# Optimization experiments

Measured on AMD Instinct MI355X. Metric: run time of the kernel, lower is better.

## Reference

```python
import jax, jax.numpy as jnp
import numpy as np

N, E, IN, HID, H, C, L, G = 20000, 640000, 128, 256, 8, 32, 5, 64
NEG_SLOPE = 0.2


def _layernorm(x, g, b, eps=1e-5):
    mu = jnp.mean(x, axis=-1, keepdims=True)
    var = jnp.mean((x - mu) ** 2, axis=-1, keepdims=True)
    return (x - mu) * jax.lax.rsqrt(var + eps) * g + b


def _gatv2(h, src, dst, Wl, bl, Wr, br, att, out_bias):
    # h: [N, HID]; src/dst: [E+N] (self loops appended)
    n = h.shape[0]
    xl = (h @ Wl + bl).reshape(n, H, C)  # source transform
    xr = (h @ Wr + br).reshape(n, H, C)  # target transform
    e = jax.nn.leaky_relu(xl[src] + xr[dst], NEG_SLOPE)       # [Etot, H, C]
    logits = jnp.einsum('ehc,hc->eh', e, att)                  # [Etot, H]
    m = jax.ops.segment_max(logits, dst, num_segments=n)       # segment softmax over dst
    a = jnp.exp(logits - m[dst])
    s = jax.ops.segment_sum(a, dst, num_segments=n)
    alpha = a / (s[dst] + 1e-16)                               # [Etot, H]
    out = jax.ops.segment_sum(alpha[:, :, None] * xl[src], dst, num_segments=n)
    return out.reshape(n, HID) + out_bias


def setup_inputs() -> dict:
    key = jax.random.key(0)
    ks = jax.random.split(key, 16)
    sc = 0.05
    inp = {
        'x': jax.random.normal(ks[0], (N, IN), jnp.float32),
        'edge_index': jax.random.randint(ks[1], (2, E), 0, N, jnp.int64),
        'batch': jnp.sort(jax.random.randint(ks[2], (N,), 0, G, jnp.int64)),
        'proj_W': jax.random.normal(ks[3], (IN, HID), jnp.float32) * sc,
        'proj_b': jnp.zeros((HID,), jnp.float32),
        'Wl': jax.random.normal(ks[4], (L, HID, HID), jnp.float32) * sc,
        'bl': jnp.zeros((L, HID), jnp.float32),
        'Wr': jax.random.normal(ks[5], (L, HID, HID), jnp.float32) * sc,
        'br': jnp.zeros((L, HID), jnp.float32),
        'att': jax.random.normal(ks[6], (L, H, C), jnp.float32) * sc,
        'out_bias': jnp.zeros((L, HID), jnp.float32),
        'ln_g': jnp.ones((L, HID), jnp.float32),
        'ln_b': jnp.zeros((L, HID), jnp.float32),
    }
    return inp


def reference(x, edge_index, batch, proj_W, proj_b, Wl, bl, Wr, br, att, out_bias, ln_g, ln_b):
    n = x.shape[0]
    loops = jnp.arange(n, dtype=edge_index.dtype)
    src = jnp.concatenate([edge_index[0], loops])  # add_self_loops=True
    dst = jnp.concatenate([edge_index[1], loops])
    h = x @ proj_W + proj_b
    for i in range(L):  # dropout = identity in eval mode
        conv = _gatv2(h, src, dst, Wl[i], bl[i], Wr[i], br[i], att[i], out_bias[i])
        h = _layernorm(h + jax.nn.elu(conv), ln_g[i], ln_b[i])
    counts = jax.ops.segment_sum(jnp.ones((n,), h.dtype), batch, num_segments=G)
    gsum = jax.ops.segment_sum(h, batch, num_segments=G)
    graph_emb = gsum / jnp.maximum(counts, 1.0)[:, None]  # global_mean_pool
    return graph_emb, h, batch
```

## Files before the change

### kernel.cpp

```cpp
#include <hip/hip_runtime.h>
#include <hip/hip_bf16.h>

#define NN   20000
#define NE   640000
#define INF_ 128
#define HID  256
#define NL   5
#define NG   64

typedef __hip_bfloat16 bf16;
typedef __attribute__((ext_vector_type(4))) float f32x4;
typedef __attribute__((ext_vector_type(8))) short bf16x8;

#if __has_builtin(__builtin_amdgcn_exp2f)
#define EXP2F __builtin_amdgcn_exp2f
#else
#define EXP2F exp2f
#endif

__device__ __forceinline__ float b2f(bf16 v) { return __bfloat162float(v); }
__device__ __forceinline__ short f2bs(float v) {
  union { bf16 h; short s; } u; u.h = __float2bfloat16(v); return u.s;
}
__device__ __forceinline__ f32x4 ldbf4o(const char* __restrict__ basep, unsigned off) {
  const uint2 u = *(const uint2*)(basep + off);
  f32x4 r;
  r[0] = __uint_as_float(u.x << 16);
  r[1] = __uint_as_float(u.x & 0xffff0000u);
  r[2] = __uint_as_float(u.y << 16);
  r[3] = __uint_as_float(u.y & 0xffff0000u);
  return r;
}

#if __has_builtin(__builtin_amdgcn_update_dpp)
template<int CTRL>
__device__ __forceinline__ float dpp_add(float v) {
  int t = __builtin_amdgcn_update_dpp(0, __float_as_int(v), CTRL, 0xF, 0xF, true);
  return v + __int_as_float(t);
}
__device__ __forceinline__ float hsum8(float v) {
  v = dpp_add<0xB1>(v);
  v = dpp_add<0x4E>(v);
  v = dpp_add<0x141>(v);
  return v;
}
__device__ __forceinline__ float wsum64(float v) {
  v = hsum8(v);
  v = dpp_add<0x140>(v);
  v += __shfl_xor(v, 16);
  v += __shfl_xor(v, 32);
  return v;
}
#else
__device__ __forceinline__ float hsum8(float v) {
  v += __shfl_xor(v, 1);  v += __shfl_xor(v, 2);  v += __shfl_xor(v, 4);
  return v;
}
__device__ __forceinline__ float wsum64(float v) {
  v += __shfl_xor(v, 1);  v += __shfl_xor(v, 2);  v += __shfl_xor(v, 4);
  v += __shfl_xor(v, 8);  v += __shfl_xor(v, 16); v += __shfl_xor(v, 32);
  return v;
}
#endif

__global__ void detect_kernel(const int* __restrict__ ei,
                              const int* __restrict__ batch,
                              int* __restrict__ flags) {
  if (blockIdx.x == 0) {
    const int k = threadIdx.x;
    const bool e_bad = (k < 40) && (ei[2 * (k * 15999) + 1] != 0);
    const bool b_bad = (k < 40) && (batch[2 * (k * 249) + 1] != 0);
    const int e64 = __any(e_bad) ? 0 : 1;
    const int b64 = __any(b_bad) ? 0 : 1;
    if (k == 0) { flags[0] = e64; flags[1] = b64; }
  }
}

__device__ __forceinline__ int ld_i(const int* p, int f, size_t idx) {
  return f ? p[2 * idx] : p[idx];
}

__global__ void hist_kernel(const int* __restrict__ ei, const int* __restrict__ flags,
                            int* __restrict__ deg) {
  int e = blockIdx.x * blockDim.x + threadIdx.x;
  if (e >= NE) return;
  int f = flags[0];
  int d = ld_i(ei, f, (size_t)NE + e);
  if ((unsigned)d < NN) atomicAdd(&deg[d], 1);
}

#define SCAN_NB ((NN + 255) / 256)
__global__ __launch_bounds__(256) void scan1_kernel(
    const int* __restrict__ deg, int* __restrict__ off, int* __restrict__ bsum)
{
  __shared__ int sh[256];
  const int t = threadIdx.x;
  const int i = blockIdx.x * 256 + t;
  const int v = (i < NN) ? deg[i] : 0;
  sh[t] = v;
  __syncthreads();
  for (int d = 1; d < 256; d <<= 1) {
    int nv = (t >= d) ? sh[t - d] : 0;
    __syncthreads();
    sh[t] += nv;
    __syncthreads();
  }
  if (i < NN) off[i] = sh[t] - v;
  if (t == 255) bsum[blockIdx.x] = sh[255];
}

__global__ __launch_bounds__(128) void scan2_kernel(
    const int* __restrict__ bsum, int* __restrict__ boff, int* __restrict__ off)
{
  __shared__ int sh[128];
  const int t = threadIdx.x;
  const int v = (t < SCAN_NB) ? bsum[t] : 0;
  sh[t] = v;
  __syncthreads();
  for (int d = 1; d < 128; d <<= 1) {
    int nv = (t >= d) ? sh[t - d] : 0;
    __syncthreads();
    sh[t] += nv;
    __syncthreads();
  }
  if (t < SCAN_NB) boff[t] = sh[t] - v;
  if (t == SCAN_NB - 1) off[NN] = sh[t];
}

__global__ __launch_bounds__(256) void scan3_kernel(
    int* __restrict__ off, const int* __restrict__ boff, int* __restrict__ tmp)
{
  const int i = blockIdx.x * 256 + threadIdx.x;
  if (i < NN) {
    const int val = off[i] + boff[blockIdx.x];
    off[i] = val;
    tmp[i] = val;
  }
}

__global__ void scatter_kernel(const int* __restrict__ ei, const int* __restrict__ flags,
                               int* __restrict__ tmp, int* __restrict__ csr) {
  int e = blockIdx.x * blockDim.x + threadIdx.x;
  if (e >= NE) return;
  int f = flags[0];
  int d = ld_i(ei, f, (size_t)NE + e);
  int s = ld_i(ei, f, (size_t)e);
  if ((unsigned)d < NN) {
    int p = atomicAdd(&tmp[d], 1);
    int sv = ((unsigned)s < NN) ? s : 0;
    if ((unsigned)p < NE) csr[p] = sv * (HID * 2);
  }
}

__global__ __launch_bounds__(256) void prep_bt_kernel(
    const float* __restrict__ projW, const float* __restrict__ Wl,
    const float* __restrict__ Wr, short* __restrict__ BTp,
    short* __restrict__ BTl, short* __restrict__ BTr)
{
  __shared__ float t[32][33];
  const int z = blockIdx.z;
  const float* src; short* dst; int K;
  if (z == 0)      { src = projW;                            dst = BTp;                              K = INF_; }
  else if (z <= NL){ src = Wl + (size_t)(z - 1) * HID * HID; dst = BTl + (size_t)(z - 1) * HID * HID; K = HID; }
  else             { src = Wr + (size_t)(z - 1 - NL) * HID * HID; dst = BTr + (size_t)(z - 1 - NL) * HID * HID; K = HID; }
  const int k0 = blockIdx.y * 32;
  if (k0 >= K) return;
  const int n0 = blockIdx.x * 32;
  const int tx = threadIdx.x & 31;
  const int ty = threadIdx.x >> 5;
#pragma unroll
  for (int i = 0; i < 32; i += 8)
    t[ty + i][tx] = src[(size_t)(k0 + ty + i) * HID + n0 + tx];
  __syncthreads();
#pragma unroll
  for (int i = 0; i < 32; i += 8)
    dst[(size_t)(n0 + ty + i) * K + k0 + tx] = f2bs(t[tx][ty + i]);
}

template<int K, bool A_BF16>
__global__ __launch_bounds__(256) void gemm_bias_kernel(
    const void* __restrict__ Av, const float* __restrict__ B,
    const float* __restrict__ bias, float* __restrict__ Cf,
    bf16* __restrict__ Cb, int M)
{
  constexpr int N = 256;
  constexpr int LDB = K + 8;
  __shared__ __align__(16) short bT[32 * LDB];
  const int tid = threadIdx.x;
  const int n0 = blockIdx.x * 32;
  const int m_base = blockIdx.y * 256;

  if (tid < K) {
    const float* brow = B + (size_t)tid * N + n0;
#pragma unroll
    for (int j = 0; j < 32; ++j) bT[j * LDB + tid] = f2bs(brow[j]);
  }
  __syncthreads();

  const int wave = tid >> 6;
  const int lane = tid & 63;
  const int r    = lane & 15;
  const int quad = lane >> 4;
  const int m_wave = m_base + wave * 64;

  f32x4 acc[4][2];
#pragma unroll
  for (int i = 0; i < 4; ++i) { acc[i][0] = (f32x4)0.0f; acc[i][1] = (f32x4)0.0f; }

#pragma unroll
  for (int kk = 0; kk < K / 32; ++kk) {
    const int kof = kk * 32 + quad * 8;
    bf16x8 b0 = *(const bf16x8*)&bT[r * LDB + kof];
    bf16x8 b1 = *(const bf16x8*)&bT[(r + 16) * LDB + kof];
#pragma unroll
    for (int sm = 0; sm < 4; ++sm) {
      const int row = m_wave + sm * 16 + r;
      bf16x8 a = (bf16x8)(short)0;
      if (row < M) {
        if constexpr (A_BF16) {
          a = *(const bf16x8*)((const short*)Av + (size_t)row * K + kof);
        } else {
          const float* ap = (const float*)Av + (size_t)row * K + kof;
          f32x4 lo = *(const f32x4*)ap;
          f32x4 hi = *(const f32x4*)(ap + 4);
#pragma unroll
          for (int j = 0; j < 4; ++j) { a[j] = f2bs(lo[j]); a[4 + j] = f2bs(hi[j]); }
        }
      }
      acc[sm][0] = __builtin_amdgcn_mfma_f32_16x16x32_bf16(a, b0, acc[sm][0], 0, 0, 0);
      acc[sm][1] = __builtin_amdgcn_mfma_f32_16x16x32_bf16(a, b1, acc[sm][1], 0, 0, 0);
    }
  }

  const float bv0 = bias[n0 + r];
  const float bv1 = bias[n0 + 16 + r];
#pragma unroll
  for (int sm = 0; sm < 4; ++sm) {
#pragma unroll
    for (int rg = 0; rg < 4; ++rg) {
      const int row = m_wave + sm * 16 + quad * 4 + rg;
      if (row < M) {
        size_t i0 = (size_t)row * N + n0 + r;
        float v0 = acc[sm][0][rg] + bv0;
        float v1 = acc[sm][1][rg] + bv1;
        if (Cf) { Cf[i0] = v0; Cf[i0 + 16] = v1; }
        if (Cb) {
          ((unsigned short*)Cb)[i0]      = (unsigned short)f2bs(v0);
          ((unsigned short*)Cb)[i0 + 16] = (unsigned short)f2bs(v1);
        }
      }
    }
  }
}

template<bool A_BF16>
__global__ __launch_bounds__(256) void gemm_dual_kernel(
    const void* __restrict__ Av,
    const float* __restrict__ Bl, const float* __restrict__ Br,
    const float* __restrict__ bl, const float* __restrict__ br,
    bf16* __restrict__ Cl, bf16* __restrict__ Cr, int M)
{
  constexpr int K = HID, N = 256;
  constexpr int LDB = K + 8;
  __shared__ __align__(16) short bTl[32 * LDB];
  __shared__ __align__(16) short bTr[32 * LDB];
  const int tid = threadIdx.x;
  const int n0 = blockIdx.x * 32;
  const int m_base = blockIdx.y * 256;

  {
    const float* browl = Bl + (size_t)tid * N + n0;
    const float* browr = Br + (size_t)tid * N + n0;
#pragma unroll
    for (int j = 0; j < 32; ++j) {
      bTl[j * LDB + tid] = f2bs(browl[j]);
      bTr[j * LDB + tid] = f2bs(browr[j]);
    }
  }
  __syncthreads();

  const int wave = tid >> 6;
  const int lane = tid & 63;
  const int r    = lane & 15;
  const int quad = lane >> 4;
  const int m_wave = m_base + wave * 64;

  f32x4 accl[4][2], accr[4][2];
#pragma unroll
  for (int i = 0; i < 4; ++i) {
    accl[i][0] = (f32x4)0.0f; accl[i][1] = (f32x4)0.0f;
    accr[i][0] = (f32x4)0.0f; accr[i][1] = (f32x4)0.0f;
  }

#pragma unroll
  for (int kk = 0; kk < K / 32; ++kk) {
    const int kof = kk * 32 + quad * 8;
    bf16x8 b0l = *(const bf16x8*)&bTl[r * LDB + kof];
    bf16x8 b1l = *(const bf16x8*)&bTl[(r + 16) * LDB + kof];
    bf16x8 b0r = *(const bf16x8*)&bTr[r * LDB + kof];
    bf16x8 b1r = *(const bf16x8*)&bTr[(r + 16) * LDB + kof];
#pragma unroll
    for (int sm = 0; sm < 4; ++sm) {
      const int row = m_wave + sm * 16 + r;
      bf16x8 a = (bf16x8)(short)0;
      if (row < M) {
        if constexpr (A_BF16) {
          a = *(const bf16x8*)((const short*)Av + (size_t)row * K + kof);
        } else {
          const float* ap = (const float*)Av + (size_t)row * K + kof;
          f32x4 lo = *(const f32x4*)ap;
          f32x4 hi = *(const f32x4*)(ap + 4);
#pragma unroll
          for (int j = 0; j < 4; ++j) { a[j] = f2bs(lo[j]); a[4 + j] = f2bs(hi[j]); }
        }
      }
      accl[sm][0] = __builtin_amdgcn_mfma_f32_16x16x32_bf16(a, b0l, accl[sm][0], 0, 0, 0);
      accl[sm][1] = __builtin_amdgcn_mfma_f32_16x16x32_bf16(a, b1l, accl[sm][1], 0, 0, 0);
      accr[sm][0] = __builtin_amdgcn_mfma_f32_16x16x32_bf16(a, b0r, accr[sm][0], 0, 0, 0);
      accr[sm][1] = __builtin_amdgcn_mfma_f32_16x16x32_bf16(a, b1r, accr[sm][1], 0, 0, 0);
    }
  }

  const float bl0v = bl[n0 + r],  bl1v = bl[n0 + 16 + r];
  const float br0v = br[n0 + r],  br1v = br[n0 + 16 + r];
#pragma unroll
  for (int sm = 0; sm < 4; ++sm) {
#pragma unroll
    for (int rg = 0; rg < 4; ++rg) {
      const int row = m_wave + sm * 16 + quad * 4 + rg;
      if (row < M) {
        size_t i0 = (size_t)row * N + n0 + r;
        ((unsigned short*)Cl)[i0]      = (unsigned short)f2bs(accl[sm][0][rg] + bl0v);
        ((unsigned short*)Cl)[i0 + 16] = (unsigned short)f2bs(accl[sm][1][rg] + bl1v);
        ((unsigned short*)Cr)[i0]      = (unsigned short)f2bs(accr[sm][0][rg] + br0v);
        ((unsigned short*)Cr)[i0 + 16] = (unsigned short)f2bs(accr[sm][1][rg] + br1v);
      }
    }
  }
}

__global__ __launch_bounds__(256) void gemm_dual_tiled_kernel(
    const short* __restrict__ Ab,
    const short* __restrict__ BTl, const short* __restrict__ BTr,
    const float* __restrict__ bl, const float* __restrict__ br,
    bf16* __restrict__ Cl, bf16* __restrict__ Cr, int M)
{
  constexpr int K = HID;
  __shared__ __align__(16) short bfr[32768];
  const int tid  = threadIdx.x;
  const int lane = tid & 63;
  const int wv   = tid >> 6;
  const int bx   = blockIdx.x;
  const int n0   = (bx & 1) * 128;
  const short* BT = (bx < 2) ? BTl : BTr;
  const float* bias = (bx < 2) ? bl : br;
  bf16* C = (bx < 2) ? Cl : Cr;

#pragma unroll
  for (int it = 0; it < 16; ++it) {
    const int c  = it * 256 + tid;
    const int f  = c >> 6;
    const int ln = c & 63;
    const int nf = f >> 3, kk = f & 7;
    const int rr = ln & 15, qq = ln >> 4;
    const short* src = BT + (size_t)(n0 + nf * 16 + rr) * K + kk * 32 + qq * 8;
    *(bf16x8*)&bfr[(size_t)c * 8] = *(const bf16x8*)src;
  }
  __syncthreads();

  const int r    = lane & 15;
  const int quad = lane >> 4;
  const int m_wave = blockIdx.y * 128 + wv * 32;

  f32x4 acc[2][8];
#pragma unroll
  for (int sm = 0; sm < 2; ++sm)
#pragma unroll
    for (int nf = 0; nf < 8; ++nf) acc[sm][nf] = (f32x4)0.0f;

  const int ar0 = min(m_wave + r, M - 1);
  const int ar1 = min(m_wave + 16 + r, M - 1);
  const short* a0p = Ab + (size_t)ar0 * K + quad * 8;
  const short* a1p = Ab + (size_t)ar1 * K + quad * 8;
#pragma unroll
  for (int kk = 0; kk < 8; ++kk) {
    const bf16x8 a0 = *(const bf16x8*)(a0p + kk * 32);
    const bf16x8 a1 = *(const bf16x8*)(a1p + kk * 32);
#pragma unroll
    for (int nf = 0; nf < 8; ++nf) {
      const bf16x8 b = *(const bf16x8*)&bfr[((nf * 8 + kk) * 64 + lane) * 8];
      acc[0][nf] = __builtin_amdgcn_mfma_f32_16x16x32_bf16(a0, b, acc[0][nf], 0, 0, 0);
      acc[1][nf] = __builtin_amdgcn_mfma_f32_16x16x32_bf16(a1, b, acc[1][nf], 0, 0, 0);
    }
  }

  float bv[8];
#pragma unroll
  for (int nf = 0; nf < 8; ++nf) bv[nf] = bias[n0 + nf * 16 + r];

#pragma unroll
  for (int sm = 0; sm < 2; ++sm) {
#pragma unroll
    for (int rg = 0; rg < 4; ++rg) {
      const int row = m_wave + sm * 16 + quad * 4 + rg;
      if (row < M) {
        unsigned short* cp = (unsigned short*)C + (size_t)row * 256 + n0 + r;
#pragma unroll
        for (int nf = 0; nf < 8; ++nf)
          cp[nf * 16] = (unsigned short)f2bs(acc[sm][nf][rg] + bv[nf]);
      }
    }
  }
}

__global__ __launch_bounds__(256) void gat_layer_kernel(
    const bf16* __restrict__ xl, const bf16* __restrict__ xr,
    float* __restrict__ h, bf16* __restrict__ h_bf,
    const int* __restrict__ off, const int* __restrict__ csr,
    const float* __restrict__ att, const float* __restrict__ outb,
    const float* __restrict__ lng, const float* __restrict__ lnb)
{
  const int lane = threadIdx.x & 63;
  const int node = __builtin_amdgcn_readfirstlane(blockIdx.x * 4 + (threadIdx.x >> 6));
  const int cb   = ((lane >> 3) << 5) + ((lane & 7) << 2);
  const unsigned cb2  = (unsigned)cb * 2;
  const unsigned selfo = (unsigned)node * (HID * 2) + cb2;
  const size_t base = (size_t)node * HID + cb;
  const char* xlc = (const char*)xl;

  const f32x4 xrv = ldbf4o((const char*)xr, selfo);
  const f32x4 xls = ldbf4o(xlc, selfo);
  const f32x4 av = *(const f32x4*)(att + cb);
  f32x4 a6, a4;
#pragma unroll
  for (int c = 0; c < 4; ++c) {
    a6[c] = av[c] * (0.6f * 1.44269504f);
    a4[c] = av[c] * (0.4f * 1.44269504f);
  }

  const f32x4 ob = *(const f32x4*)(outb + cb);
  const f32x4 hv = *(const f32x4*)(h + base);
  const f32x4 g4 = *(const f32x4*)(lng + cb);
  const f32x4 b4 = *(const f32x4*)(lnb + cb);

  float pa = 0.f;
#pragma unroll
  for (int c = 0; c < 4; ++c) {
    float z = xls[c] + xrv[c];
    pa = fmaf(a6[c], z, pa);
    pa = fmaf(a4[c], fabsf(z), pa);
  }
  const float es = EXP2F(hsum8(pa));
  float s = es;
  f32x4 o;
#pragma unroll
  for (int c = 0; c < 4; ++c) o[c] = es * xls[c];

  int beg = __builtin_amdgcn_readfirstlane(off[node]);
  int end = __builtin_amdgcn_readfirstlane(off[node + 1]);
  if (beg < 0) beg = 0;
  if (end > NE) end = NE;
  const unsigned* csrb = (const unsigned*)csr;

  const int nblk = (end > beg) ? ((end - beg) >> 3) : 0;
  unsigned nx[8];
  if (nblk > 0) {
#pragma unroll
    for (int j = 0; j < 8; ++j) nx[j] = csrb[beg + j];
  }
  for (int b = 0; b < nblk; ++b) {
    f32x4 xv[8];
#pragma unroll
    for (int j = 0; j < 8; ++j) xv[j] = ldbf4o(xlc, nx[j] + cb2);
    if (b + 1 < nblk) {
      const int pn = beg + (b + 1) * 8;
#pragma unroll
      for (int j = 0; j < 8; ++j) nx[j] = csrb[pn + j];
    }
    float e[8];
#pragma unroll
    for (int j = 0; j < 8; ++j) {
      float acc = 0.f;
#pragma unroll
      for (int c = 0; c < 4; ++c) {
        float z = xv[j][c] + xrv[c];
        acc = fmaf(a6[c], z, acc);
        acc = fmaf(a4[c], fabsf(z), acc);
      }
      e[j] = EXP2F(hsum8(acc));
    }
    s += (((e[0] + e[1]) + (e[2] + e[3])) + ((e[4] + e[5]) + (e[6] + e[7])));
#pragma unroll
    for (int c = 0; c < 4; ++c) {
      float c0 = fmaf(e[0], xv[0][c], fmaf(e[1], xv[1][c],
                 fmaf(e[2], xv[2][c], fmaf(e[3], xv[3][c], o[c]))));
      float c1 = fmaf(e[4], xv[4][c], fmaf(e[5], xv[5][c],
                 fmaf(e[6], xv[6][c], e[7] * xv[7][c])));
      o[c] = c0 + c1;
    }
  }
  for (int p = beg + nblk * 8; p < end; ++p) {
    const unsigned oo = csrb[p] + cb2;
    const f32x4 xv = ldbf4o(xlc, oo);
    float pe = 0.f;
#pragma unroll
    for (int c = 0; c < 4; ++c) {
      float z = xv[c] + xrv[c];
      pe = fmaf(a6[c], z, pe);
      pe = fmaf(a4[c], fabsf(z), pe);
    }
    const float ee = EXP2F(hsum8(pe));
    s += ee;
#pragma unroll
    for (int c = 0; c < 4; ++c) o[c] = fmaf(ee, xv[c], o[c]);
  }

  const float inv_s = 1.f / s;
  f32x4 res;
#pragma unroll
  for (int c = 0; c < 4; ++c) {
    float conv = fmaf(o[c], inv_s, ob[c]);
    float el = conv > 0.f ? conv : (__expf(conv) - 1.f);
    res[c] = hv[c] + el;
  }
  float pr = (res[0] + res[1]) + (res[2] + res[3]);
  const float mu = wsum64(pr) * (1.f / 256.f);
  f32x4 dv;
  float p2s = 0.f;
#pragma unroll
  for (int c = 0; c < 4; ++c) { dv[c] = res[c] - mu; p2s = fmaf(dv[c], dv[c], p2s); }
  const float var = wsum64(p2s) * (1.f / 256.f);
  const float rs = rsqrtf(var + 1e-5f);
  f32x4 y;
#pragma unroll
  for (int c = 0; c < 4; ++c) y[c] = fmaf(dv[c] * rs, g4[c], b4[c]);

  *(f32x4*)(h + base) = y;
  if (h_bf) {
    ushort4 u;
    u.x = (unsigned short)f2bs(y[0]);
    u.y = (unsigned short)f2bs(y[1]);
    u.z = (unsigned short)f2bs(y[2]);
    u.w = (unsigned short)f2bs(y[3]);
    *(ushort4*)((unsigned short*)h_bf + base) = u;
  }
}

__global__ __launch_bounds__(256) void pool_kernel(
    const float* __restrict__ h, const int* __restrict__ batch,
    const int* __restrict__ flags, float* __restrict__ gsum, int* __restrict__ gcnt)
{
  const int t = threadIdx.x;
  const int f = flags[1];
  int n0 = blockIdx.x * 80;
  int n1 = n0 + 80; if (n1 > NN) n1 = NN;
  float acc = 0.f;
  int g_cur = ld_i(batch, f, n0);
  if ((unsigned)g_cur >= NG) g_cur = 0;
  int run = 0;
  for (int n = n0; n < n1; ++n) {
    int g = ld_i(batch, f, n);
    if ((unsigned)g >= NG) g = 0;
    if (g != g_cur) {
      atomicAdd(&gsum[(size_t)g_cur * HID + t], acc);
      if (t == 0) atomicAdd(&gcnt[g_cur], run);
      acc = 0.f; run = 0; g_cur = g;
    }
    acc += h[(size_t)n * HID + t];
    ++run;
  }
  atomicAdd(&gsum[(size_t)g_cur * HID + t], acc);
  if (t == 0) atomicAdd(&gcnt[g_cur], run);
}

__global__ void write_out_kernel(const float* __restrict__ gsum, const int* __restrict__ gcnt,
                                 const int* __restrict__ batch,
                                 const int* __restrict__ flags, float* __restrict__ out)
{
  int i = blockIdx.x * blockDim.x + threadIdx.x;
  if (i < NG * HID) {
    int g = i >> 8;
    float c = (float)gcnt[g];
    c = c > 1.f ? c : 1.f;
    out[i] = gsum[i] / c;
  } else if (i < NG * HID + NN) {
    int n = i - NG * HID;
    int f = flags[1];
    out[(size_t)NG * HID + (size_t)NN * HID + n] = (float)ld_i(batch, f, (size_t)n);
  }
}

extern "C" void kernel_launch(void* const* d_in, const int* in_sizes, int n_in,
                              void* d_out, int out_size, void* d_ws, size_t ws_size,
                              hipStream_t stream) {
  (void)in_sizes; (void)n_in; (void)out_size;

  const float* x     = (const float*)d_in[0];
  const int*   ei    = (const int*)d_in[1];
  const int*   batch = (const int*)d_in[2];
  const float* projW = (const float*)d_in[3];
  const float* projB = (const float*)d_in[4];
  const float* Wl    = (const float*)d_in[5];
  const float* bl    = (const float*)d_in[6];
  const float* Wr    = (const float*)d_in[7];
  const float* br    = (const float*)d_in[8];
  const float* att   = (const float*)d_in[9];
  const float* outb  = (const float*)d_in[10];
  const float* lng   = (const float*)d_in[11];
  const float* lnb   = (const float*)d_in[12];
  float* out = (float*)d_out;

  float* h = out + (size_t)NG * HID;

  char* ws = (char*)d_ws;
  size_t o = 0;
  auto alloc = [&](size_t bytes) -> void* {
    void* p = ws + o;
    o += (bytes + 255) & ~(size_t)255;
    return p;
  };
  int*   flags = (int*)alloc(4 * 4);
  int*   deg   = (int*)alloc((size_t)NN * 4);
  int*   offs  = (int*)alloc((size_t)(NN + 1) * 4);
  int*   tmp   = (int*)alloc((size_t)NN * 4);
  float* gsum  = (float*)alloc((size_t)NG * HID * 4);
  int*   gcnt  = (int*)alloc((size_t)NG * 4);
  int*   bsum  = (int*)alloc((size_t)(SCAN_NB + 1) * 4);
  int*   boff  = (int*)alloc((size_t)(SCAN_NB + 1) * 4);
  int*   csr   = (int*)alloc((size_t)NE * 4);
  bf16*  xl    = (bf16*)alloc((size_t)NN * HID * 2);
  bf16*  xr    = (bf16*)alloc((size_t)NN * HID * 2);
  size_t o_base = o;
  bf16*  h_bf  = (bf16*)alloc((size_t)NN * HID * 2);
  const bool use_hbf = (ws_size >= o);
  if (!use_hbf) { h_bf = nullptr; o = o_base; }
  size_t o_hbf = o;
  short* BTp = (short*)alloc((size_t)HID * INF_ * 2);
  short* BTl = (short*)alloc((size_t)NL * HID * HID * 2);
  short* BTr = (short*)alloc((size_t)NL * HID * HID * 2);
  const bool use_bt = use_hbf && (ws_size >= o);
  if (!use_bt) { o = o_hbf; }

  hipMemsetAsync(deg, 0, (size_t)NN * 4, stream);
  hipMemsetAsync(gsum, 0, (size_t)NG * HID * 4 + (size_t)NG * 4, stream);

  detect_kernel<<<1, 64, 0, stream>>>(ei, batch, flags);

  if (use_bt) {
    dim3 pb(256), pg(8, 8, 2 * NL + 1);
    prep_bt_kernel<<<pg, pb, 0, stream>>>(projW, Wl, Wr, BTp, BTl, BTr);
  }

  hist_kernel<<<(NE + 255) / 256, 256, 0, stream>>>(ei, flags, deg);
  scan1_kernel<<<SCAN_NB, 256, 0, stream>>>(deg, offs, bsum);
  scan2_kernel<<<1, 128, 0, stream>>>(bsum, boff, offs);
  scan3_kernel<<<SCAN_NB, 256, 0, stream>>>(offs, boff, tmp);
  scatter_kernel<<<(NE + 255) / 256, 256, 0, stream>>>(ei, flags, tmp, csr);

  dim3 gg(HID / 32, (NN + 255) / 256);

  gemm_bias_kernel<INF_, false><<<gg, 256, 0, stream>>>(x, projW, projB, h, h_bf, NN);

  dim3 gt(4, (NN + 127) / 128);
  for (int i = 0; i < NL; ++i) {
    if (use_bt) {
      gemm_dual_tiled_kernel<<<gt, 256, 0, stream>>>((const short*)h_bf,
          BTl + (size_t)i * HID * HID, BTr + (size_t)i * HID * HID,
          bl + (size_t)i * HID, br + (size_t)i * HID, xl, xr, NN);
    } else if (use_hbf) {
      gemm_dual_kernel<true><<<gg, 256, 0, stream>>>(h_bf,
          Wl + (size_t)i * HID * HID, Wr + (size_t)i * HID * HID,
          bl + (size_t)i * HID, br + (size_t)i * HID, xl, xr, NN);
    } else {
      gemm_dual_kernel<false><<<gg, 256, 0, stream>>>(h,
          Wl + (size_t)i * HID * HID, Wr + (size_t)i * HID * HID,
          bl + (size_t)i * HID, br + (size_t)i * HID, xl, xr, NN);
    }
    gat_layer_kernel<<<NN / 4, 256, 0, stream>>>(xl, xr, h, h_bf, offs, csr,
                                                 att + (size_t)i * HID, outb + (size_t)i * HID,
                                                 lng + (size_t)i * HID, lnb + (size_t)i * HID);
  }

  pool_kernel<<<250, 256, 0, stream>>>(h, batch, flags, gsum, gcnt);
  write_out_kernel<<<(NG * HID + NN + 255) / 256, 256, 0, stream>>>(gsum, gcnt, batch, flags, out);
}
```

Before: 529.9 us.

## Pre-swizzle weights into MFMA fragment layout and double-buffer GAT neighbor gathers

The weight prep kernel now writes Wl/Wr directly in the per-lane MFMA fragment order, so the dual GEMM can fill shared memory with contiguous 16-byte copies instead of strided row reads. The GEMM also issues all A-operand loads before the barrier so they overlap the shared-memory fill. The GAT aggregation loop is restructured with two gather buffers, so the next block's neighbor features load while the current block is computed. This raises register pressure in the attention kernel and drops the unused projection weight transpose.

New measurement: 523.4 us. About the same (-1.2%).

```diff
diff --git a/kernel.cpp b/kernel.cpp
--- a/kernel.cpp
+++ b/kernel.cpp
@@ -21,15 +21,6 @@
 __device__ __forceinline__ float b2f(bf16 v) { return __bfloat162float(v); }
 __device__ __forceinline__ short f2bs(float v) {
   union { bf16 h; short s; } u; u.h = __float2bfloat16(v); return u.s;
-}
-__device__ __forceinline__ f32x4 ldbf4o(const char* __restrict__ basep, unsigned off) {
-  const uint2 u = *(const uint2*)(basep + off);
-  f32x4 r;
-  r[0] = __uint_as_float(u.x << 16);
-  r[1] = __uint_as_float(u.x & 0xffff0000u);
-  r[2] = __uint_as_float(u.y << 16);
-  r[3] = __uint_as_float(u.y & 0xffff0000u);
-  return r;
 }
 
 #if __has_builtin(__builtin_amdgcn_update_dpp)
@@ -152,29 +143,26 @@
   }
 }
 
-__global__ __launch_bounds__(256) void prep_bt_kernel(
-    const float* __restrict__ projW, const float* __restrict__ Wl,
-    const float* __restrict__ Wr, short* __restrict__ BTp,
+__global__ __launch_bounds__(256) void prep_btf_kernel(
+    const float* __restrict__ Wl, const float* __restrict__ Wr,
     short* __restrict__ BTl, short* __restrict__ BTr)
 {
-  __shared__ float t[32][33];
-  const int z = blockIdx.z;
-  const float* src; short* dst; int K;
-  if (z == 0)      { src = projW;                            dst = BTp;                              K = INF_; }
-  else if (z <= NL){ src = Wl + (size_t)(z - 1) * HID * HID; dst = BTl + (size_t)(z - 1) * HID * HID; K = HID; }
-  else             { src = Wr + (size_t)(z - 1 - NL) * HID * HID; dst = BTr + (size_t)(z - 1 - NL) * HID * HID; K = HID; }
-  const int k0 = blockIdx.y * 32;
-  if (k0 >= K) return;
-  const int n0 = blockIdx.x * 32;
-  const int tx = threadIdx.x & 31;
-  const int ty = threadIdx.x >> 5;
-#pragma unroll
-  for (int i = 0; i < 32; i += 8)
-    t[ty + i][tx] = src[(size_t)(k0 + ty + i) * HID + n0 + tx];
-  __syncthreads();
-#pragma unroll
-  for (int i = 0; i < 32; i += 8)
-    dst[(size_t)(n0 + ty + i) * K + k0 + tx] = f2bs(t[tx][ty + i]);
+  const int z = blockIdx.y;
+  const float* src = (z < NL) ? Wl + (size_t)z * HID * HID
+                              : Wr + (size_t)(z - NL) * HID * HID;
+  short* dst = (z < NL) ? BTl + (size_t)z * HID * HID
+                        : BTr + (size_t)(z - NL) * HID * HID;
+  const int g = blockIdx.x * 256 + threadIdx.x;
+  const int ln   = g & 63;
+  const int frag = (g >> 6) & 63;
+  const int half = g >> 12;
+  const int nf = frag >> 3, kk = frag & 7;
+  const int n  = half * 128 + nf * 16 + (ln & 15);
+  const int k0 = kk * 32 + (ln >> 4) * 8;
+  bf16x8 outv;
+#pragma unroll
+  for (int j = 0; j < 8; ++j) outv[j] = f2bs(src[(size_t)(k0 + j) * HID + n]);
+  *(bf16x8*)&dst[(size_t)g * 8] = outv;
 }
 
 template<int K, bool A_BF16>
@@ -352,45 +340,47 @@
   const int wv   = tid >> 6;
   const int bx   = blockIdx.x;
   const int n0   = (bx & 1) * 128;
-  const short* BT = (bx < 2) ? BTl : BTr;
+  const short* BTf = (bx < 2) ? BTl : BTr;
   const float* bias = (bx < 2) ? bl : br;
   bf16* C = (bx < 2) ? Cl : Cr;
+  const short* src = BTf + (size_t)(bx & 1) * 32768;
 
 #pragma unroll
   for (int it = 0; it < 16; ++it) {
-    const int c  = it * 256 + tid;
-    const int f  = c >> 6;
-    const int ln = c & 63;
-    const int nf = f >> 3, kk = f & 7;
-    const int rr = ln & 15, qq = ln >> 4;
-    const short* src = BT + (size_t)(n0 + nf * 16 + rr) * K + kk * 32 + qq * 8;
-    *(bf16x8*)&bfr[(size_t)c * 8] = *(const bf16x8*)src;
-  }
-  __syncthreads();
+    const int c = it * 256 + tid;
+    *(bf16x8*)&bfr[(size_t)c * 8] = *(const bf16x8*)&src[(size_t)c * 8];
+  }
 
   const int r    = lane & 15;
   const int quad = lane >> 4;
   const int m_wave = blockIdx.y * 128 + wv * 32;
-
-  f32x4 acc[2][8];
-#pragma unroll
-  for (int sm = 0; sm < 2; ++sm)
-#pragma unroll
-    for (int nf = 0; nf < 8; ++nf) acc[sm][nf] = (f32x4)0.0f;
 
   const int ar0 = min(m_wave + r, M - 1);
   const int ar1 = min(m_wave + 16 + r, M - 1);
   const short* a0p = Ab + (size_t)ar0 * K + quad * 8;
   const short* a1p = Ab + (size_t)ar1 * K + quad * 8;
+  bf16x8 a0[8], a1[8];
 #pragma unroll
   for (int kk = 0; kk < 8; ++kk) {
-    const bf16x8 a0 = *(const bf16x8*)(a0p + kk * 32);
-    const bf16x8 a1 = *(const bf16x8*)(a1p + kk * 32);
+    a0[kk] = *(const bf16x8*)(a0p + kk * 32);
+    a1[kk] = *(const bf16x8*)(a1p + kk * 32);
+  }
+
+  __syncthreads();
+
+  f32x4 acc[2][8];
+#pragma unroll
+  for (int sm = 0; sm < 2; ++sm)
+#pragma unroll
+    for (int nf = 0; nf < 8; ++nf) acc[sm][nf] = (f32x4)0.0f;
+
+#pragma unroll
+  for (int kk = 0; kk < 8; ++kk) {
 #pragma unroll
     for (int nf = 0; nf < 8; ++nf) {
       const bf16x8 b = *(const bf16x8*)&bfr[((nf * 8 + kk) * 64 + lane) * 8];
-      acc[0][nf] = __builtin_amdgcn_mfma_f32_16x16x32_bf16(a0, b, acc[0][nf], 0, 0, 0);
-      acc[1][nf] = __builtin_amdgcn_mfma_f32_16x16x32_bf16(a1, b, acc[1][nf], 0, 0, 0);
+      acc[0][nf] = __builtin_amdgcn_mfma_f32_16x16x32_bf16(a0[kk], b, acc[0][nf], 0, 0, 0);
+      acc[1][nf] = __builtin_amdgcn_mfma_f32_16x16x32_bf16(a1[kk], b, acc[1][nf], 0, 0, 0);
     }
   }
 
@@ -428,8 +418,14 @@
   const size_t base = (size_t)node * HID + cb;
   const char* xlc = (const char*)xl;
 
-  const f32x4 xrv = ldbf4o((const char*)xr, selfo);
-  const f32x4 xls = ldbf4o(xlc, selfo);
+  const uint2 uxr = *(const uint2*)((const char*)xr + selfo);
+  const uint2 uxl = *(const uint2*)(xlc + selfo);
+  f32x4 xrv, xls;
+  xrv[0] = __uint_as_float(uxr.x << 16); xrv[1] = __uint_as_float(uxr.x & 0xffff0000u);
+  xrv[2] = __uint_as_float(uxr.y << 16); xrv[3] = __uint_as_float(uxr.y & 0xffff0000u);
+  xls[0] = __uint_as_float(uxl.x << 16); xls[1] = __uint_as_float(uxl.x & 0xffff0000u);
+  xls[2] = __uint_as_float(uxl.y << 16); xls[3] = __uint_as_float(uxl.y & 0xffff0000u);
+
   const f32x4 av = *(const f32x4*)(att + cb);
   f32x4 a6, a4;
 #pragma unroll
@@ -463,19 +459,27 @@
   const unsigned* csrb = (const unsigned*)csr;
 
   const int nblk = (end > beg) ? ((end - beg) >> 3) : 0;
-  unsigned nx[8];
-  if (nblk > 0) {
-#pragma unroll
-    for (int j = 0; j < 8; ++j) nx[j] = csrb[beg + j];
-  }
-  for (int b = 0; b < nblk; ++b) {
+
+  unsigned adr[8];
+  uint2 bufA[8], bufB[8];
+
+  auto LOADADR = [&](int blk) {
+    const int pp = beg + blk * 8;
+#pragma unroll
+    for (int j = 0; j < 8; ++j) adr[j] = csrb[pp + j];
+  };
+  auto GATHER = [&](uint2 (&buf)[8]) {
+#pragma unroll
+    for (int j = 0; j < 8; ++j) buf[j] = *(const uint2*)(xlc + (adr[j] + cb2));
+  };
+  auto COMPUTE = [&](const uint2 (&buf)[8]) {
     f32x4 xv[8];
 #pragma unroll
-    for (int j = 0; j < 8; ++j) xv[j] = ldbf4o(xlc, nx[j] + cb2);
-    if (b + 1 < nblk) {
-      const int pn = beg + (b + 1) * 8;
-#pragma unroll
-      for (int j = 0; j < 8; ++j) nx[j] = csrb[pn + j];
+    for (int j = 0; j < 8; ++j) {
+      xv[j][0] = __uint_as_float(buf[j].x << 16);
+      xv[j][1] = __uint_as_float(buf[j].x & 0xffff0000u);
+      xv[j][2] = __uint_as_float(buf[j].y << 16);
+      xv[j][3] = __uint_as_float(buf[j].y & 0xffff0000u);
     }
     float e[8];
 #pragma unroll
@@ -498,10 +502,32 @@
                  fmaf(e[6], xv[6][c], e[7] * xv[7][c])));
       o[c] = c0 + c1;
     }
-  }
+  };
+
+  if (nblk > 0) {
+    LOADADR(0);
+    GATHER(bufA);
+    if (nblk > 1) LOADADR(1);
+  }
+  int b = 0;
+  for (; b + 2 <= nblk; b += 2) {
+    GATHER(bufB);
+    if (b + 2 < nblk) LOADADR(b + 2);
+    COMPUTE(bufA);
+    if (b + 2 < nblk) {
+      GATHER(bufA);
+      if (b + 3 < nblk) LOADADR(b + 3);
+    }
+    COMPUTE(bufB);
+  }
+  if (b < nblk) COMPUTE(bufA);
+
   for (int p = beg + nblk * 8; p < end; ++p) {
     const unsigned oo = csrb[p] + cb2;
-    const f32x4 xv = ldbf4o(xlc, oo);
+    const uint2 u = *(const uint2*)(xlc + oo);
+    f32x4 xv;
+    xv[0] = __uint_as_float(u.x << 16); xv[1] = __uint_as_float(u.x & 0xffff0000u);
+    xv[2] = __uint_as_float(u.y << 16); xv[3] = __uint_as_float(u.y & 0xffff0000u);
     float pe = 0.f;
 #pragma unroll
     for (int c = 0; c < 4; ++c) {
@@ -635,7 +661,6 @@
   const bool use_hbf = (ws_size >= o);
   if (!use_hbf) { h_bf = nullptr; o = o_base; }
   size_t o_hbf = o;
-  short* BTp = (short*)alloc((size_t)HID * INF_ * 2);
   short* BTl = (short*)alloc((size_t)NL * HID * HID * 2);
   short* BTr = (short*)alloc((size_t)NL * HID * HID * 2);
   const bool use_bt = use_hbf && (ws_size >= o);
@@ -647,8 +672,8 @@
   detect_kernel<<<1, 64, 0, stream>>>(ei, batch, flags);
 
   if (use_bt) {
-    dim3 pb(256), pg(8, 8, 2 * NL + 1);
-    prep_bt_kernel<<<pg, pb, 0, stream>>>(projW, Wl, Wr, BTp, BTl, BTr);
+    dim3 pg(32, 2 * NL);
+    prep_btf_kernel<<<pg, 256, 0, stream>>>(Wl, Wr, BTl, BTr);
   }
 
   hist_kernel<<<(NE + 255) / 256, 256, 0, stream>>>(ei, flags, deg);
```
